# Kernel tuning notes

Hardware: AMD Instinct MI355X
Metric: run time of the kernel (lower is better)

Reference implementation:

```python
import jax, jax.numpy as jnp
import numpy as np

EMBED = 512
HEADS = 8
DIM_HEAD = 64          # embed_dim // 8
LANDMARKS = 256        # embed_dim // 2
PINV_ITERS = 6
RES_K = 33             # nystrom residual_conv_kernel default
SCALE = DIM_HEAD ** -0.5


def layer_norm(x, g, b, eps=1e-5):
    mu = x.mean(-1, keepdims=True)
    var = ((x - mu) ** 2).mean(-1, keepdims=True)
    return (x - mu) / jnp.sqrt(var + eps) * g + b


def moore_penrose_pinv(x, iters=PINV_ITERS):
    # iterative Moore-Penrose pseudo-inverse (lucidrains nystrom-attention)
    ax = jnp.abs(x)
    z = jnp.swapaxes(x, -1, -2) / (ax.sum(-1).max() * ax.sum(-2).max())
    I = jnp.eye(x.shape[-1], dtype=x.dtype)
    for _ in range(iters):
        xz = x @ z
        z = 0.25 * z @ (13. * I - xz @ (15. * I - xz @ (7. * I - xz)))
    return z


def nystrom_attention(x, w_qkv, w_out, b_out, res_k):
    b, n, _ = x.shape
    m = LANDMARKS
    pad = (m - n % m) % m
    xp = jnp.pad(x, ((0, 0), (pad, 0), (0, 0)))  # left-pad like F.pad(..., padding, 0)
    np_ = n + pad
    qkv = (xp @ w_qkv).reshape(b, np_, 3, HEADS, DIM_HEAD)
    q = qkv[:, :, 0].transpose(0, 2, 1, 3) * SCALE   # [b,h,np,dh]
    k = qkv[:, :, 1].transpose(0, 2, 1, 3)
    v = qkv[:, :, 2].transpose(0, 2, 1, 3)
    l = np_ // m
    q_l = q.reshape(b, HEADS, m, l, DIM_HEAD).mean(3)  # [b,h,m,dh]
    k_l = k.reshape(b, HEADS, m, l, DIM_HEAD).mean(3)
    attn1 = jax.nn.softmax(jnp.einsum('bhid,bhjd->bhij', q, k_l), -1)    # [b,h,np,m]
    attn2 = jax.nn.softmax(jnp.einsum('bhid,bhjd->bhij', q_l, k_l), -1)  # [b,h,m,m]
    attn3 = jax.nn.softmax(jnp.einsum('bhid,bhjd->bhij', q_l, k), -1)    # [b,h,m,np]
    out = (attn1 @ moore_penrose_pinv(attn2)) @ (attn3 @ v)              # [b,h,np,dh]
    # depthwise residual conv over the sequence dim, per head (shared across dh)
    v_c = v.transpose(0, 3, 1, 2).reshape(b * DIM_HEAD, HEADS, np_)
    res = jax.lax.conv_general_dilated(
        v_c, res_k[:, None, :], (1,), [(RES_K // 2, RES_K // 2)],
        dimension_numbers=('NCH', 'OIH', 'NCH'), feature_group_count=HEADS)
    out = out + res.reshape(b, DIM_HEAD, HEADS, np_).transpose(0, 2, 3, 1)
    out = out.transpose(0, 2, 1, 3).reshape(b, np_, HEADS * DIM_HEAD)
    out = out @ w_out + b_out
    return out[:, -n:]  # drop left padding


def dwconv2d(x, w, b, k):
    # x: [B,C,H,W], w: [C,1,k,k] depthwise
    y = jax.lax.conv_general_dilated(
        x, w, (1, 1), [(k // 2, k // 2)] * 2,
        dimension_numbers=('NCHW', 'OIHW', 'NCHW'), feature_group_count=x.shape[1])
    return y + b[None, :, None, None]


def ppeg(x, H, W, w7, b7, w5, b5, w3, b3):
    B, _, C = x.shape
    cls_tok, feat = x[:, :1], x[:, 1:]
    f = feat.transpose(0, 2, 1).reshape(B, C, H, W)
    y = f + dwconv2d(f, w7, b7, 7) + dwconv2d(f, w5, b5, 5) + dwconv2d(f, w3, b3, 3)
    y = y.reshape(B, C, H * W).transpose(0, 2, 1)
    return jnp.concatenate([cls_tok, y], axis=1)


def reference(h, w_fc1, b_fc1, cls_token,
              ln1_g, ln1_b, qkv1_w, out1_w, out1_b, res1_k,
              conv7_w, conv7_b, conv5_w, conv5_b, conv3_w, conv3_b,
              ln2_g, ln2_b, qkv2_w, out2_w, out2_b, res2_k,
              lnf_g, lnf_b):
    h = jax.nn.relu(h @ w_fc1 + b_fc1)                 # [B,N,512]
    B, N, C = h.shape
    _H = int(np.ceil(np.sqrt(N)))
    add = _H * _H - N
    h = jnp.concatenate([h, h[:, :add]], axis=1)       # square padding
    h = jnp.concatenate([jnp.broadcast_to(cls_token, (B, 1, C)), h], axis=1)
    h = h + nystrom_attention(layer_norm(h, ln1_g, ln1_b), qkv1_w, out1_w, out1_b, res1_k)
    h = ppeg(h, _H, _H, conv7_w, conv7_b, conv5_w, conv5_b, conv3_w, conv3_b)
    h = h + nystrom_attention(layer_norm(h, ln2_g, ln2_b), qkv2_w, out2_w, out2_b, res2_k)
    return layer_norm(h, lnf_g, lnf_b)[:, 0]           # [B,512]


def setup_inputs() -> dict:
    key = jax.random.key(0)
    ks = jax.random.split(key, 24)
    B, N, IN_DIM = 2, 4096, 1024
    w = lambda k, shape, s=0.02: jax.random.normal(k, shape, jnp.float32) * s
    z = lambda shape: jnp.zeros(shape, jnp.float32)
    o = lambda shape: jnp.ones(shape, jnp.float32)
    return {
        'h': jax.random.normal(ks[0], (B, N, IN_DIM), jnp.float32),
        'w_fc1': w(ks[1], (IN_DIM, EMBED)), 'b_fc1': z((EMBED,)),
        'cls_token': w(ks[2], (1, 1, EMBED)),
        'ln1_g': o((EMBED,)), 'ln1_b': z((EMBED,)),
        'qkv1_w': w(ks[3], (EMBED, 3 * HEADS * DIM_HEAD)),
        'out1_w': w(ks[4], (HEADS * DIM_HEAD, EMBED)), 'out1_b': z((EMBED,)),
        'res1_k': w(ks[5], (HEADS, RES_K), 0.1),
        'conv7_w': w(ks[6], (EMBED, 1, 7, 7), 0.05), 'conv7_b': z((EMBED,)),
        'conv5_w': w(ks[7], (EMBED, 1, 5, 5), 0.05), 'conv5_b': z((EMBED,)),
        'conv3_w': w(ks[8], (EMBED, 1, 3, 3), 0.05), 'conv3_b': z((EMBED,)),
        'ln2_g': o((EMBED,)), 'ln2_b': z((EMBED,)),
        'qkv2_w': w(ks[9], (EMBED, 3 * HEADS * DIM_HEAD)),
        'out2_w': w(ks[10], (HEADS * DIM_HEAD, EMBED)), 'out2_b': z((EMBED,)),
        'res2_k': w(ks[11], (HEADS, RES_K), 0.1),
        'lnf_g': o((EMBED,)), 'lnf_b': z((EMBED,)),
    }
```

## Files before the change

### kernel.cpp

```cpp
#include <hip/hip_runtime.h>
#include <hip/hip_bf16.h>

#define HEADS 8
#define DH 64
#define EMB 512
#define NP 4352
#define NTOK 4097
#define PADF 255
#define LM 256
#define SCALE 0.125f

typedef __attribute__((ext_vector_type(8))) short bf8;
typedef __attribute__((ext_vector_type(4))) float f4;
typedef __attribute__((ext_vector_type(8))) unsigned short us8;
typedef __attribute__((ext_vector_type(4))) unsigned short us4;
typedef unsigned short u16;

__device__ __forceinline__ u16 f2b(float f){
  union { float f; unsigned u; } x; x.f = f;
  unsigned r = x.u + 0x7fffu + ((x.u>>16)&1u);
  return (u16)(r>>16);
}
__device__ __forceinline__ float b2f(u16 h){
  union { unsigned u; float f; } x; x.u = ((unsigned)h)<<16;
  return x.f;
}

__device__ __forceinline__ void gload_lds(const u16* g, u16* l){
  __builtin_amdgcn_global_load_lds((const __attribute__((address_space(1))) void*)g,
                                   (__attribute__((address_space(3))) void*)l, 16, 0, 0);
}

template<int MODE>
__global__ __launch_bounds__(256)
void k_g128(const u16* __restrict__ A, const u16* __restrict__ B,
            float* __restrict__ C, u16* __restrict__ C16,
            int K, int lda, int ldb, int ldc,
            long sAb, long sAh, long sBb, long sBh, long sCb, long sCh, int nh,
            float alpha, const float* __restrict__ bias, int relu, int rowoff,
            int nx, int ksplit)
{
  int z = blockIdx.z;
  const u16* Ab = A + (long)(z/nh)*sAb + (long)(z%nh)*sAh;
  const u16* Bb = B + (long)(z/nh)*sBb + (long)(z%nh)*sBh;
  long cb = (long)(z/nh)*sCb + (long)(z%nh)*sCh;
  int bx = blockIdx.x % nx, kc = blockIdx.x / nx;
  int m0 = blockIdx.y*128, n0 = bx*128;
  int klen = K/ksplit, kbeg = kc*klen, nch = klen/32;
  __shared__ u16 As[2][4096];
  __shared__ u16 Bs[2][4096];
  int tid=threadIdx.x, w=tid>>6, lane=tid&63, q=lane>>4, lr=lane&15;
  int wrow=(w>>1)*64, wcol=(w&1)*64;
  int srow = tid>>2, scol = (tid&3)*8;
  const u16* ga  = Ab + (long)(m0+srow)*lda + kbeg + scol;
  const u16* ga2 = Ab + (long)(m0+64+srow)*lda + kbeg + scol;
  const u16* gb  = Bb + (long)(n0+srow)*ldb + kbeg + scol;
  const u16* gb2 = Bb + (long)(n0+64+srow)*ldb + kbeg + scol;
  int lo = srow*32 + scol;
  f4 acc[4][4] = {};
  auto stage = [&](int r, int c){
    gload_lds(ga  + c*32, &As[r][lo]);
    gload_lds(ga2 + c*32, &As[r][2048+lo]);
    gload_lds(gb  + c*32, &Bs[r][lo]);
    gload_lds(gb2 + c*32, &Bs[r][2048+lo]);
  };
  auto compute = [&](int r){
    bf8 af[4], bfr[4];
    #pragma unroll
    for(int rr=0;rr<4;rr++) af[rr]  = *(const bf8*)&As[r][(wrow + rr*16 + lr)*32 + q*8];
    #pragma unroll
    for(int t=0;t<4;t++) bfr[t] = *(const bf8*)&Bs[r][(wcol + t*16 + lr)*32 + q*8];
    #pragma unroll
    for(int rr=0;rr<4;rr++)
      #pragma unroll
      for(int t=0;t<4;t++)
        acc[rr][t] = __builtin_amdgcn_mfma_f32_16x16x32_bf16(af[rr], bfr[t], acc[rr][t], 0,0,0);
  };
  stage(0,0);
  __syncthreads();
  for(int c=1;c<nch;c++){
    stage(c&1, c);
    compute((c-1)&1);
    __syncthreads();
  }
  compute((nch-1)&1);
  #pragma unroll
  for(int r=0;r<4;r++){
    #pragma unroll
    for(int t=0;t<4;t++){
      #pragma unroll
      for(int e=0;e<4;e++){
        int gm = m0 + wrow + r*16 + q*4 + e;
        int gn = n0 + wcol + t*16 + lr;
        float v = acc[r][t][e]*alpha;
        if(MODE==4){
          if(bias && kc==0) v += bias[gn];
          if(gm>=rowoff) atomicAdd(&C[cb + (long)(gm-rowoff)*ldc + gn], v);
        } else {
          if(bias) v += bias[gn];
          if(relu) v = fmaxf(v,0.f);
          if(MODE==0) C[cb + (long)gm*ldc + gn] = v;
          else if(MODE==2) C16[cb + (long)gm*ldc + gn] = f2b(v);
          else { if(gm>=rowoff) C[cb + (long)(gm-rowoff)*ldc + gn] += v; }
        }
      }
    }
  }
}

template<int MODE>
__global__ __launch_bounds__(256)
void k_g64(const u16* __restrict__ A, const u16* __restrict__ B,
           float* __restrict__ C, u16* __restrict__ C16,
           int K, int lda, int ldb, int ldc,
           long sAb, long sAh, long sBb, long sBh, long sCb, long sCh, int nh,
           float alpha, const float* __restrict__ bias, int rowoff, int moff,
           int nx, int ksplit)
{
  int z = blockIdx.z;
  const u16* Ab = A + (long)(z/nh)*sAb + (long)(z%nh)*sAh;
  const u16* Bb = B + (long)(z/nh)*sBb + (long)(z%nh)*sBh;
  long cb = (long)(z/nh)*sCb + (long)(z%nh)*sCh;
  int bx = blockIdx.x % nx, kc = blockIdx.x / nx;
  int m0 = blockIdx.y*64 + moff, n0 = bx*64;
  int klen = K/ksplit, kbeg = kc*klen, nch = klen/32;
  __shared__ u16 As[2][2048];
  __shared__ u16 Bs[2][2048];
  int tid=threadIdx.x, w=tid>>6, lane=tid&63, q=lane>>4, lr=lane&15;
  int srow = tid>>2, scol = (tid&3)*8;
  const u16* ga = Ab + (long)(m0+srow)*lda + kbeg + scol;
  const u16* gb = Bb + (long)(n0+srow)*ldb + kbeg + scol;
  int lo = srow*32 + scol;
  f4 acc[4] = {};
  auto stage = [&](int r, int c){
    gload_lds(ga + c*32, &As[r][lo]);
    gload_lds(gb + c*32, &Bs[r][lo]);
  };
  auto compute = [&](int r){
    bf8 af = *(const bf8*)&As[r][(w*16 + lr)*32 + q*8];
    #pragma unroll
    for(int t=0;t<4;t++){
      bf8 bfr = *(const bf8*)&Bs[r][(t*16 + lr)*32 + q*8];
      acc[t] = __builtin_amdgcn_mfma_f32_16x16x32_bf16(af, bfr, acc[t], 0,0,0);
    }
  };
  stage(0,0);
  __syncthreads();
  for(int c=1;c<nch;c++){
    stage(c&1, c);
    compute((c-1)&1);
    __syncthreads();
  }
  compute((nch-1)&1);
  #pragma unroll
  for(int t=0;t<4;t++){
    #pragma unroll
    for(int e=0;e<4;e++){
      int gm = m0 + w*16 + q*4 + e;
      int gn = n0 + t*16 + lr;
      float v = acc[t][e]*alpha;
      if(MODE==0) C[cb + (long)gm*ldc + gn] = v;
      else if(MODE==2) C16[cb + (long)gm*ldc + gn] = f2b(v);
      else if(MODE==3) atomicAdd(&C[cb + (long)gm*ldc + gn], v);
      else if(MODE==5){
        v += bias[gn];
        if(gm>=rowoff) C[cb + (long)(gm-rowoff)*ldc + gn] += v;
      }
    }
  }
}

__global__ __launch_bounds__(256)
void k_pg3(const u16* __restrict__ Ah, const u16* __restrict__ Al,
           const u16* __restrict__ Bh, const u16* __restrict__ Bl,
           u16* __restrict__ Oh, u16* __restrict__ Ol, float na, float nd,
           u16* __restrict__ TOh, u16* __restrict__ TOl, float ta, float td)
{
  long zo = (long)blockIdx.z*65536;
  int m0 = blockIdx.y*32, n0 = blockIdx.x*64;
  __shared__ u16 S[2][6144];
  int tid=threadIdx.x, w=tid>>6, lane=tid&63, q=lane>>4, lr=lane&15;
  int t2 = tid & 127;
  const u16* srcA = (tid<128 ? Ah : Al) + zo + (long)(m0 + (t2>>2))*256 + (t2&3)*8;
  const u16* srcBh = Bh + zo + (long)(n0 + (tid>>2))*256 + (tid&3)*8;
  const u16* srcBl = Bl + zo + (long)(n0 + (tid>>2))*256 + (tid&3)*8;
  f4 acc[2] = {};
  auto stage = [&](int r, int c){
    gload_lds(srcA  + c*32, &S[r][tid*8]);
    gload_lds(srcBh + c*32, &S[r][2048 + tid*8]);
    gload_lds(srcBl + c*32, &S[r][4096 + tid*8]);
  };
  int mrow = (w>>1)*16 + lr;
  auto compute = [&](int r){
    bf8 ah = *(const bf8*)&S[r][mrow*32 + q*8];
    bf8 al = *(const bf8*)&S[r][1024 + mrow*32 + q*8];
    #pragma unroll
    for(int t=0;t<2;t++){
      int nrow = (w&1)*32 + t*16 + lr;
      bf8 bh = *(const bf8*)&S[r][2048 + nrow*32 + q*8];
      bf8 bl = *(const bf8*)&S[r][4096 + nrow*32 + q*8];
      acc[t] = __builtin_amdgcn_mfma_f32_16x16x32_bf16(ah, bh, acc[t], 0,0,0);
      acc[t] = __builtin_amdgcn_mfma_f32_16x16x32_bf16(ah, bl, acc[t], 0,0,0);
      acc[t] = __builtin_amdgcn_mfma_f32_16x16x32_bf16(al, bh, acc[t], 0,0,0);
    }
  };
  stage(0,0);
  __syncthreads();
  #pragma unroll
  for(int c=1;c<8;c++){
    stage(c&1, c);
    compute((c-1)&1);
    __syncthreads();
  }
  compute(1);
  #pragma unroll
  for(int t=0;t<2;t++){
    int gn = n0 + (w&1)*32 + t*16 + lr;
    if(Oh){
      #pragma unroll
      for(int r=0;r<4;r++){
        int gm = m0 + (w>>1)*16 + q*4 + r;
        float v = na*acc[t][r] + ((gm==gn)?nd:0.f);
        u16 h = f2b(v);
        long o = zo + (long)gm*256 + gn;
        Oh[o] = h; Ol[o] = f2b(v - b2f(h));
      }
    }
    if(TOh){
      us4 th, tl;
      #pragma unroll
      for(int r=0;r<4;r++){
        int gm = m0 + (w>>1)*16 + q*4 + r;
        float v = ta*acc[t][r] + ((gm==gn)?td:0.f);
        u16 h = f2b(v);
        th[r] = h; tl[r] = f2b(v - b2f(h));
      }
      long o = zo + (long)gn*256 + (m0 + (w>>1)*16 + q*4);
      *(us4*)&TOh[o] = th; *(us4*)&TOl[o] = tl;
    }
  }
}

__global__ __launch_bounds__(256)
void k_att1(const u16* __restrict__ qkv16, const u16* __restrict__ kl,
            const u16* __restrict__ zavT, float* __restrict__ Qc)
{
  int z = blockIdx.y, b = z>>3, h = z&7;
  int m0 = blockIdx.x*64;
  __shared__ u16 SQ[64*64];
  __shared__ u16 SKL[256*64];
  __shared__ u16 SZV[64*256];
  int tid=threadIdx.x, w=tid>>6, lane=tid&63, q=lane>>4, lr=lane&15;
  {
    const u16* qb = qkv16 + (long)b*NP*1536 + h*64;
    #pragma unroll
    for(int p=0;p<2;p++){
      int idx = tid + p*256; int row = idx>>3, c8 = (idx&7)*8;
      gload_lds(qb + (long)(m0+row)*1536 + c8, &SQ[row*64 + c8]);
    }
    const u16* kb = kl + (long)z*16384;
    #pragma unroll
    for(int p=0;p<8;p++){
      int idx = tid + p*256; int row = idx>>3, c8 = (idx&7)*8;
      gload_lds(kb + row*64 + c8, &SKL[row*64 + c8]);
    }
    const u16* zb = zavT + (long)z*16384;
    #pragma unroll
    for(int p=0;p<8;p++){
      int idx = tid + p*256; int row = idx>>5, c8 = (idx&31)*8;
      gload_lds(zb + row*256 + c8, &SZV[row*256 + c8]);
    }
  }
  __syncthreads();
  f4 acc[16] = {};
  {
    bf8 af0 = *(const bf8*)&SQ[(w*16+lr)*64 + q*8];
    bf8 af1 = *(const bf8*)&SQ[(w*16+lr)*64 + 32 + q*8];
    #pragma unroll
    for(int t=0;t<16;t++){
      bf8 b0 = *(const bf8*)&SKL[(t*16+lr)*64 + q*8];
      bf8 b1 = *(const bf8*)&SKL[(t*16+lr)*64 + 32 + q*8];
      acc[t] = __builtin_amdgcn_mfma_f32_16x16x32_bf16(af0, b0, acc[t], 0,0,0);
      acc[t] = __builtin_amdgcn_mfma_f32_16x16x32_bf16(af1, b1, acc[t], 0,0,0);
    }
  }
  float mx[4] = {-1e30f,-1e30f,-1e30f,-1e30f};
  #pragma unroll
  for(int t=0;t<16;t++)
    #pragma unroll
    for(int e=0;e<4;e++) mx[e] = fmaxf(mx[e], acc[t][e]*SCALE);
  #pragma unroll
  for(int s=1;s<16;s<<=1)
    #pragma unroll
    for(int e=0;e<4;e++) mx[e] = fmaxf(mx[e], __shfl_xor(mx[e], s));
  float sm[4] = {0.f,0.f,0.f,0.f};
  #pragma unroll
  for(int t=0;t<16;t++)
    #pragma unroll
    for(int e=0;e<4;e++){ float p = expf(acc[t][e]*SCALE - mx[e]); acc[t][e]=p; sm[e]+=p; }
  #pragma unroll
  for(int s=1;s<16;s<<=1)
    #pragma unroll
    for(int e=0;e<4;e++) sm[e] += __shfl_xor(sm[e], s);
  float inv[4];
  #pragma unroll
  for(int e=0;e<4;e++) inv[e] = 1.f/sm[e];
  __syncthreads();
  u16* PS = SKL;
  #pragma unroll
  for(int t=0;t<16;t++)
    #pragma unroll
    for(int e=0;e<4;e++)
      PS[(w*16 + q*4 + e)*256 + t*16 + lr] = f2b(acc[t][e]*inv[e]);
  __syncthreads();
  f4 acc2[4] = {};
  #pragma unroll
  for(int ks=0;ks<8;ks++){
    bf8 af = *(const bf8*)&PS[(w*16+lr)*256 + ks*32 + q*8];
    #pragma unroll
    for(int t=0;t<4;t++){
      bf8 bf_ = *(const bf8*)&SZV[(t*16+lr)*256 + ks*32 + q*8];
      acc2[t] = __builtin_amdgcn_mfma_f32_16x16x32_bf16(af, bf_, acc2[t], 0,0,0);
    }
  }
  #pragma unroll
  for(int t=0;t<4;t++)
    #pragma unroll
    for(int r=0;r<4;r++){
      int gm = m0 + w*16 + q*4 + r;
      int gd = t*16 + lr;
      Qc[((long)b*NP + gm)*512 + h*64 + gd] = acc2[t][r];
    }
}

__global__ __launch_bounds__(256)
void k_smw32(float* __restrict__ X){
  long row = (long)blockIdx.x*4 + (threadIdx.x>>6);
  int lane = threadIdx.x & 63;
  float* p = X + row*256;
  float4 v = *(float4*)&p[lane*4];
  float m = fmaxf(fmaxf(v.x,v.y),fmaxf(v.z,v.w));
  for(int s=32;s;s>>=1) m = fmaxf(m, __shfl_xor(m, s));
  float e0=expf(v.x-m), e1=expf(v.y-m), e2=expf(v.z-m), e3=expf(v.w-m);
  float sum = e0+e1+e2+e3;
  for(int s=32;s;s>>=1) sum += __shfl_xor(sum, s);
  float inv = 1.f/sum;
  float4 o = {e0*inv, e1*inv, e2*inv, e3*inv};
  *(float4*)&p[lane*4] = o;
}

__global__ __launch_bounds__(256)
void k_smb16(u16* __restrict__ X){
  u16* p = X + (long)blockIdx.x*4352;
  int tid=threadIdx.x, lane=tid&63, w=tid>>6;
  __shared__ float xw[4], sw[4];
  float e[17];
  float m = -1e30f;
  #pragma unroll
  for(int i=0;i<17;i++){ e[i] = b2f(p[tid + i*256]); m = fmaxf(m, e[i]); }
  for(int s=32;s;s>>=1) m = fmaxf(m, __shfl_xor(m, s));
  if(lane==0) xw[w] = m;
  __syncthreads();
  m = fmaxf(fmaxf(xw[0],xw[1]), fmaxf(xw[2],xw[3]));
  float sum = 0.f;
  #pragma unroll
  for(int i=0;i<17;i++){ e[i] = expf(e[i]-m); sum += e[i]; }
  for(int s=32;s;s>>=1) sum += __shfl_xor(sum, s);
  if(lane==0) sw[w] = sum;
  __syncthreads();
  sum = sw[0]+sw[1]+sw[2]+sw[3];
  float inv = 1.f/sum;
  #pragma unroll
  for(int i=0;i<17;i++) p[tid + i*256] = f2b(e[i]*inv);
}

__global__ void k_wT(const float* __restrict__ in, u16* __restrict__ out, int K, int N){
  int n0=blockIdx.x*32, k0=blockIdx.y*32, tid=threadIdx.x;
  __shared__ float T[32][33];
  int lr=tid&31, lc=tid>>5;
  #pragma unroll
  for(int p=0;p<4;p++) T[lc+8*p][lr] = in[(long)(k0+lc+8*p)*N + n0+lr];
  __syncthreads();
  #pragma unroll
  for(int p=0;p<4;p++) out[(long)(n0+lc+8*p)*K + k0+lr] = f2b(T[lr][lc+8*p]);
}

__global__ __launch_bounds__(256)
void k_vT(const u16* __restrict__ qkv16, u16* __restrict__ vT){
  int t0=blockIdx.x*64, h=blockIdx.y, b=blockIdx.z, tid=threadIdx.x;
  __shared__ u16 T[64][72];
  const u16* src = qkv16 + (long)b*NP*1536 + 1024 + h*64;
  for(int s=0;s<2;s++){
    int idx=tid+s*256; int row=idx>>3, c8=(idx&7)*8;
    *(us8*)&T[row][c8] = *(const us8*)&src[(long)(t0+row)*1536 + c8];
  }
  __syncthreads();
  u16* dst = vT + ((long)(b*8+h)*64)*NP;
  int d = tid>>2, j0=(tid&3)*16;
  us8 v0,v1;
  #pragma unroll
  for(int jj=0;jj<8;jj++){ v0[jj]=T[j0+jj][d]; v1[jj]=T[j0+8+jj][d]; }
  *(us8*)&dst[(long)d*NP + t0 + j0]     = v0;
  *(us8*)&dst[(long)d*NP + t0 + j0 + 8] = v1;
}

__global__ void k_cvt16(const float* __restrict__ in, u16* __restrict__ out, long n){
  long i = (long)blockIdx.x*256 + threadIdx.x;
  if(i<n) out[i] = f2b(in[i]);
}

__global__ void k_zero(float* __restrict__ p, long n){
  long i = (long)blockIdx.x*256 + threadIdx.x;
  if(i<n) p[i] = 0.f;
}

__global__ void k_cls(const float* __restrict__ cls, float* __restrict__ seq){
  int b = blockIdx.x;
  seq[(long)b*NTOK*EMB + threadIdx.x] = cls[threadIdx.x];
}

__global__ void k_ln_pad(const float* __restrict__ seq, u16* __restrict__ xp,
                         const float* __restrict__ g, const float* __restrict__ bb){
  int b = blockIdx.y, i = blockIdx.x, tid = threadIdx.x;
  u16* out = xp + ((long)b*NP + i)*EMB;
  if(i < PADF){ out[tid]=0; out[tid+256]=0; return; }
  const float* x = seq + ((long)b*NTOK + (i-PADF))*EMB;
  float v0 = x[tid], v1 = x[tid+256];
  __shared__ float red[256];
  red[tid]=v0+v1; __syncthreads();
  for(int s=128;s>0;s>>=1){ if(tid<s) red[tid]+=red[tid+s]; __syncthreads(); }
  float mu = red[0]*(1.0f/512.0f); __syncthreads();
  float d0=v0-mu, d1=v1-mu;
  red[tid]=d0*d0+d1*d1; __syncthreads();
  for(int s=128;s>0;s>>=1){ if(tid<s) red[tid]+=red[tid+s]; __syncthreads(); }
  float rstd = rsqrtf(red[0]*(1.0f/512.0f) + 1e-5f);
  out[tid]     = f2b(d0*rstd*g[tid]     + bb[tid]);
  out[tid+256] = f2b(d1*rstd*g[tid+256] + bb[tid+256]);
}

__global__ void k_landmarks(const u16* __restrict__ qkv, u16* __restrict__ q_l, u16* __restrict__ k_l){
  int j = blockIdx.x, h = blockIdx.y, b = blockIdx.z, d = threadIdx.x;
  const u16* base = qkv + (long)b*NP*1536 + h*64 + d;
  float sq=0.f, sk=0.f;
  for(int l=0;l<17;l++){
    long row = (long)(j*17+l)*1536;
    sq += b2f(base[row]);
    sk += b2f(base[row+512]);
  }
  long o = (((long)b*HEADS + h)*LM + j)*DH + d;
  q_l[o] = f2b(sq * (SCALE/17.0f));
  k_l[o] = f2b(sk * (1.0f/17.0f));
}

__global__ void k_pinv_norm(const float* __restrict__ A2, float* __restrict__ rmax, float* __restrict__ cmax){
  int z = blockIdx.x, tid = threadIdx.x;
  const float* X = A2 + (long)z*65536;
  float rs=0.f, cs=0.f;
  for(int j=0;j<256;j++){ rs += fabsf(X[tid*256+j]); cs += fabsf(X[j*256+tid]); }
  __shared__ float r1[256], r2[256];
  r1[tid]=rs; r2[tid]=cs; __syncthreads();
  for(int s=128;s>0;s>>=1){ if(tid<s){ r1[tid]=fmaxf(r1[tid],r1[tid+s]); r2[tid]=fmaxf(r2[tid],r2[tid+s]); } __syncthreads(); }
  if(tid==0){ rmax[z]=r1[0]; cmax[z]=r2[0]; }
}

__global__ void k_pair_init(const float* __restrict__ att2,
    const float* __restrict__ rmax, const float* __restrict__ cmax,
    u16* __restrict__ Xh, u16* __restrict__ Xl,
    u16* __restrict__ Zh, u16* __restrict__ Zl,
    u16* __restrict__ Zth, u16* __restrict__ Ztl)
{
  long zo = (long)blockIdx.z*65536;
  int i0 = blockIdx.y*64, j0 = blockIdx.x*64;
  float rm=0.f, cm=0.f;
  for(int t=0;t<16;t++){ rm=fmaxf(rm,rmax[t]); cm=fmaxf(cm,cmax[t]); }
  float inv = 1.0f/(rm*cm);
  __shared__ float T[64][68];
  int tid = threadIdx.x;
  int li = tid>>2, jc = (tid&3)*16;
  #pragma unroll
  for(int u=0;u<4;u++){
    float4 v = *(const float4*)&att2[zo + (long)(i0+li)*256 + j0 + jc + u*4];
    T[li][jc+u*4]=v.x; T[li][jc+u*4+1]=v.y; T[li][jc+u*4+2]=v.z; T[li][jc+u*4+3]=v.w;
    long o = zo + (long)(i0+li)*256 + j0 + jc + u*4;
    float vv[4] = {v.x,v.y,v.z,v.w};
    us4 xh, xl, zth, ztl;
    #pragma unroll
    for(int c=0;c<4;c++){
      u16 h = f2b(vv[c]); xh[c]=h; xl[c]=f2b(vv[c]-b2f(h));
      float zt = vv[c]*inv;
      u16 h2 = f2b(zt); zth[c]=h2; ztl[c]=f2b(zt-b2f(h2));
    }
    *(us4*)&Xh[o]=xh; *(us4*)&Xl[o]=xl; *(us4*)&Zth[o]=zth; *(us4*)&Ztl[o]=ztl;
  }
  __syncthreads();
  int lj = tid>>2, ic = (tid&3)*16;
  #pragma unroll
  for(int r=0;r<16;r++){
    float x = T[ic+r][lj]*inv;
    u16 h = f2b(x);
    long o = zo + (long)(j0+lj)*256 + i0 + ic + r;
    Zh[o]=h; Zl[o]=f2b(x-b2f(h));
  }
}

__global__ __launch_bounds__(256)
void k_rconv(const u16* __restrict__ qkv16, const float* __restrict__ resk,
             const float* __restrict__ Qin, u16* __restrict__ Qo16){
  int t0 = blockIdx.x*64, h = blockIdx.y, b = blockIdx.z;
  __shared__ float V[96*64];
  const u16* vb = qkv16 + (long)b*NP*1536 + 1024 + h*64;
  int tid = threadIdx.x;
  #pragma unroll
  for(int s=0;s<3;s++){
    int idx = tid + s*256;
    int row = idx>>3, c8 = (idx&7)*8;
    int p = t0 - 16 + row;
    if(p>=0 && p<NP){
      us8 v = *(const us8*)&vb[(long)p*1536 + c8];
      #pragma unroll
      for(int jj=0;jj<8;jj++) V[row*64+c8+jj] = b2f(v[jj]);
    } else {
      #pragma unroll
      for(int jj=0;jj<8;jj++) V[row*64+c8+jj] = 0.f;
    }
  }
  __syncthreads();
  int d = tid&63, lt = (tid>>6)*16;
  float acc[16] = {};
  #pragma unroll
  for(int s=0;s<48;s++){
    float val = V[(lt+s)*64 + d];
    #pragma unroll
    for(int j=0;j<16;j++){
      int tap = s - j;
      if(tap>=0 && tap<33) acc[j] += resk[h*33+tap]*val;
    }
  }
  #pragma unroll
  for(int j=0;j<16;j++){
    long idx = ((long)b*NP + t0 + lt + j)*EMB + h*64 + d;
    Qo16[idx] = f2b(Qin[idx] + acc[j]);
  }
}

__global__ __launch_bounds__(256)
void k_ppeg(const float* __restrict__ seq, float* __restrict__ out,
    const float* __restrict__ w7,const float* __restrict__ b7,
    const float* __restrict__ w5,const float* __restrict__ b5,
    const float* __restrict__ w3,const float* __restrict__ b3){
  int b = blockIdx.z, cg = blockIdx.y;
  int rp = blockIdx.x>>1, xs = blockIdx.x&1;
  int ch0 = cg*64;
  __shared__ float s7[64*49], s5[64*25], s3[64*9], sbias[64];
  int tid = threadIdx.x;
  for(int i=tid;i<64*49;i+=256) s7[i] = w7[ch0*49+i];
  for(int i=tid;i<64*25;i+=256) s5[i] = w5[ch0*25+i];
  for(int i=tid;i<64*9;i+=256)  s3[i] = w3[ch0*9+i];
  if(tid<64) sbias[tid] = b7[ch0+tid]+b5[ch0+tid]+b3[ch0+tid];
  if(cg==0 && blockIdx.x==0){
    out[(long)b*NTOK*EMB + tid]       = seq[(long)b*NTOK*EMB + tid];
    out[(long)b*NTOK*EMB + 256 + tid] = seq[(long)b*NTOK*EMB + 256 + tid];
  }
  __syncthreads();
  int c = tid & 63;
  int y = rp*4 + (tid>>6);
  const float* sbase = seq + (long)b*NTOK*EMB + EMB + (ch0 + c);
  float* obase = out + (long)b*NTOK*EMB + EMB + (ch0 + c);
  const float* W7 = &s7[c*49];
  const float* W5 = &s5[c*25];
  const float* W3 = &s3[c*9];
  float bsum = sbias[c];
  for(int xc=0;xc<4;xc++){
    int xb = xs*32 + xc*8;
    float acc[8];
    #pragma unroll
    for(int j=0;j<8;j++) acc[j] = sbase[(long)(y*64+xb+j)*EMB] + bsum;
    #pragma unroll
    for(int dy=-3;dy<=3;dy++){
      int yy = y+dy;
      if(yy<0||yy>=64) continue;
      float v[14];
      #pragma unroll
      for(int u=0;u<14;u++){
        int xx = xb + u - 3;
        v[u] = (xx>=0 && xx<64) ? sbase[(long)(yy*64+xx)*EMB] : 0.f;
      }
      #pragma unroll
      for(int dx=-3;dx<=3;dx++){
        float wsum = W7[(dy+3)*7+(dx+3)];
        if(dy>=-2&&dy<=2&&dx>=-2&&dx<=2) wsum += W5[(dy+2)*5+(dx+2)];
        if(dy>=-1&&dy<=1&&dx>=-1&&dx<=1) wsum += W3[(dy+1)*3+(dx+1)];
        #pragma unroll
        for(int j=0;j<8;j++) acc[j] += v[j+dx+3]*wsum;
      }
    }
    #pragma unroll
    for(int j=0;j<8;j++) obase[(long)(y*64+xb+j)*EMB] = acc[j];
  }
}

__global__ void k_final_ln(const float* __restrict__ seq, const float* __restrict__ g,
                           const float* __restrict__ bb, float* __restrict__ out){
  int b = blockIdx.x, tid = threadIdx.x;
  const float* x = seq + (long)b*NTOK*EMB;
  float v0 = x[tid], v1 = x[tid+256];
  __shared__ float red[256];
  red[tid]=v0+v1; __syncthreads();
  for(int s=128;s>0;s>>=1){ if(tid<s) red[tid]+=red[tid+s]; __syncthreads(); }
  float mu = red[0]*(1.0f/512.0f); __syncthreads();
  float d0=v0-mu, d1=v1-mu;
  red[tid]=d0*d0+d1*d1; __syncthreads();
  for(int s=128;s>0;s>>=1){ if(tid<s) red[tid]+=red[tid+s]; __syncthreads(); }
  float rstd = rsqrtf(red[0]*(1.0f/512.0f) + 1e-5f);
  out[b*512+tid]     = d0*rstd*g[tid]     + bb[tid];
  out[b*512+tid+256] = d1*rstd*g[tid+256] + bb[tid+256];
}

extern "C" void kernel_launch(void* const* d_in, const int* in_sizes, int n_in,
                              void* d_out, int out_size, void* d_ws, size_t ws_size,
                              hipStream_t stream) {
  const float* in[24];
  for(int i=0;i<24;i++) in[i] = (const float*)d_in[i];

  float* W = (float*)d_ws;
  size_t off = 0;
  float* seqA = W+off; off += 4195328;
  float* seqB = W+off; off += 4195328;
  float* att2 = W+off; off += 1048576;
  float* Qc   = W+off; off += 4456448;
  float* avbT = W+off; off += 262144;
  u16* xpb    = (u16*)(W+off); off += 2228224;
  u16* qkvb16 = (u16*)(W+off); off += 6684672;
  u16* vT16   = (u16*)(W+off); off += 2228224;
  u16* q_l16  = (u16*)(W+off); off += 131072;
  u16* k_l16  = (u16*)(W+off); off += 131072;
  u16* sc16   = (u16*)(W+off); off += 8912896;
  u16* avbT16 = (u16*)(W+off); off += 131072;
  u16* zavT16 = (u16*)(W+off); off += 131072;
  u16* Qc16   = (u16*)(W+off); off += 2228224;
  u16* qkvwT1 = (u16*)(W+off); off += 393216;
  u16* qkvwT2 = (u16*)(W+off); off += 393216;
  u16* outwT1 = (u16*)(W+off); off += 131072;
  u16* outwT2 = (u16*)(W+off); off += 131072;
  u16* pairs  = (u16*)(W+off); off += 9437184;
  float* rmax = W+off; off += 16;
  float* cmax = W+off; off += 16;
  if (ws_size < off*sizeof(float)) return;

  u16* h16   = sc16;
  u16* wfc1T = sc16 + 8388608;

  const long PB = 1048576;
  u16 *Xh=pairs, *Xl=pairs+PB;
  u16 *Z0h=pairs+2*PB, *Z0l=pairs+3*PB, *Z0th=pairs+4*PB, *Z0tl=pairs+5*PB;
  u16 *Z1h=pairs+6*PB, *Z1l=pairs+7*PB, *Z1th=pairs+8*PB, *Z1tl=pairs+9*PB;
  u16 *Ph=pairs+10*PB, *Pl=pairs+11*PB;
  u16 *Tth=pairs+12*PB, *Ttl=pairs+13*PB;
  u16 *Uth=pairs+14*PB, *Utl=pairs+15*PB;
  u16 *Vth=pairs+16*PB, *Vtl=pairs+17*PB;

  k_cvt16<<<32768,256,0,stream>>>(in[0], h16, 8388608L);
  k_wT<<<dim3(16,32),256,0,stream>>>(in[1],  wfc1T, 1024, 512);
  k_wT<<<dim3(48,16),256,0,stream>>>(in[6],  qkvwT1, 512, 1536);
  k_wT<<<dim3(48,16),256,0,stream>>>(in[18], qkvwT2, 512, 1536);
  k_wT<<<dim3(16,16),256,0,stream>>>(in[7],  outwT1, 512, 512);
  k_wT<<<dim3(16,16),256,0,stream>>>(in[19], outwT2, 512, 512);

  k_g128<0><<<dim3(4,32,2),256,0,stream>>>(h16, wfc1T, seqA+EMB, nullptr,
      1024, 1024,1024,512, 4194304L,0, 0,0, (long)NTOK*EMB,0, 1, 1.0f, in[2], 1, 0, 4, 1);
  k_cls<<<2,512,0,stream>>>(in[3], seqA);

  auto attention = [&](float* seq, const float* lng,const float* lnb,
                       const u16* qkvwT, const u16* outwT, const float* outb, const float* resk){
    k_ln_pad<<<dim3(NP,2),256,0,stream>>>(seq, xpb, lng, lnb);
    k_g128<2><<<dim3(12,34,2),256,0,stream>>>(xpb, qkvwT, nullptr, qkvb16,
        512, 512,512,1536, (long)NP*512,0, 0,0, (long)NP*1536,0, 1, 1.0f, nullptr, 0, 0, 12, 1);
    k_landmarks<<<dim3(LM,HEADS,2),64,0,stream>>>(qkvb16, q_l16, k_l16);
    k_vT<<<dim3(68,8,2),256,0,stream>>>(qkvb16, vT16);
    k_g128<0><<<dim3(2,2,16),256,0,stream>>>(q_l16, k_l16, att2, nullptr,
        64, 64,64,256, 0,16384, 0,16384, 0,65536, 16, 1.0f, nullptr, 0, 0, 2, 1);
    k_smw32<<<1024,256,0,stream>>>(att2);
    k_pinv_norm<<<16,256,0,stream>>>(att2, rmax, cmax);
    k_pair_init<<<dim3(4,4,16),256,0,stream>>>(att2, rmax, cmax, Xh,Xl, Z0h,Z0l, Z0th,Z0tl);
    dim3 pgrid(4,8,16);
    for(int it=0; it<6; it++){
      u16 *Zh_=(it&1)?Z1h:Z0h, *Zl_=(it&1)?Z1l:Z0l, *Zth_=(it&1)?Z1th:Z0th, *Ztl_=(it&1)?Z1tl:Z0tl;
      u16 *Nh_=(it&1)?Z0h:Z1h, *Nl_=(it&1)?Z0l:Z1l, *Nth_=(it&1)?Z0th:Z1th, *Ntl_=(it&1)?Z0tl:Z1tl;
      k_pg3<<<pgrid,256,0,stream>>>(Xh,Xl, Zth_,Ztl_, Ph,Pl,1.0f,0.f, Tth,Ttl,-1.0f,7.f);
      k_pg3<<<pgrid,256,0,stream>>>(Ph,Pl, Tth,Ttl, nullptr,nullptr,0.f,0.f, Uth,Utl,-1.0f,15.f);
      k_pg3<<<pgrid,256,0,stream>>>(Ph,Pl, Uth,Utl, nullptr,nullptr,0.f,0.f, Vth,Vtl,-1.0f,13.f);
      if(it<5) k_pg3<<<pgrid,256,0,stream>>>(Zh_,Zl_, Vth,Vtl, Nh_,Nl_,0.25f,0.f, Nth_,Ntl_,0.25f,0.f);
      else     k_pg3<<<pgrid,256,0,stream>>>(Zh_,Zl_, Vth,Vtl, Nh_,Nl_,0.25f,0.f, nullptr,nullptr,0.f,0.f);
    }
    k_g128<2><<<dim3(34,2,16),256,0,stream>>>(q_l16, qkvb16+512, nullptr, sc16,
        64, 64,1536,4352, 131072L,16384, (long)NP*1536,64, 8L*LM*NP,(long)LM*NP, 8, 1.0f, nullptr, 0, 0, 34, 1);
    k_smb16<<<4096,256,0,stream>>>(sc16);
    k_zero<<<1024,256,0,stream>>>(avbT, 262144L);
    k_g64<3><<<dim3(4*17,1,16),256,0,stream>>>(vT16, sc16, avbT, nullptr,
        4352, 4352,4352,256, 2228224L,278528L, 8L*LM*NP,(long)LM*NP, 131072L,16384L, 8, 1.0f, nullptr, 0, 0, 4, 17);
    k_cvt16<<<1024,256,0,stream>>>(avbT, avbT16, 262144L);
    k_g64<2><<<dim3(4,1,16),256,0,stream>>>(avbT16, Z0h, nullptr, zavT16,
        256, 256,256,256, 0,16384L, 0,65536L, 0,16384L, 16, 1.0f, nullptr, 0, 0, 4, 1);
    k_att1<<<dim3(68,16),256,0,stream>>>(qkvb16, k_l16, zavT16, Qc);
    k_rconv<<<dim3(68,8,2),256,0,stream>>>(qkvb16, resk, Qc, Qc16);
    k_g64<5><<<dim3(8,65,2),256,0,stream>>>(Qc16, outwT, seq, nullptr,
        512, 512,512,512, (long)NP*512,0, 0,0, (long)NTOK*EMB,0, 1, 1.0f, outb, PADF, 192, 8, 1);
  };

  attention(seqA, in[4], in[5], qkvwT1, outwT1, in[8], in[9]);
  k_ppeg<<<dim3(32,8,2),256,0,stream>>>(seqA, seqB, in[10],in[11],in[12],in[13],in[14],in[15]);
  attention(seqB, in[16], in[17], qkvwT2, outwT2, in[20], in[21]);
  k_final_ln<<<2,256,0,stream>>>(seqB, in[22], in[23], (float*)d_out);
}
```

Before: 1.039 ms.

## Fuse attn3 score, softmax and V product into split-K flash-style kernel

Replaces the materialized landmark-query × key score matrix, its separate softmax, the zeroing, the atomic-style split GEMM with V and the float-to-bf16 conversion with a single online-softmax kernel. It processes 4 key chunks in parallel per head and merges their partial results in a small merge kernel. This removes the write and re-read of the large bf16 score buffer and several launches. In exchange the fused kernel has small 128-thread blocks and a modest grid, and it adds a partial-output buffer and a merge pass. The workspace is reshuffled, and the input conversion buffers now alias the pairs region.

After: 1.025 ms. About the same (-1.4%).

```diff
diff --git a/kernel.cpp b/kernel.cpp
--- a/kernel.cpp
+++ b/kernel.cpp
@@ -241,6 +241,149 @@
   }
 }
 
+__global__ __launch_bounds__(128)
+void k_att3(const u16* __restrict__ qkv16, const u16* __restrict__ ql,
+            const u16* __restrict__ vT, float* __restrict__ partO,
+            float* __restrict__ pm, float* __restrict__ pl)
+{
+  int kc = blockIdx.x, jt = blockIdx.y, z = blockIdx.z;
+  int b = z>>3, h = z&7;
+  __shared__ u16 SQ[32*64];
+  __shared__ u16 SK[2][64*64];
+  __shared__ u16 SV[2][64*64];
+  __shared__ u16 SP[32*64];
+  int tid=threadIdx.x, w=tid>>6, lane=tid&63, q=lane>>4, lr=lane&15;
+  const u16* kb = qkv16 + (long)b*NP*1536 + 512 + h*64;
+  const u16* vb = vT + (long)z*64*NP;
+  int t00 = kc*1088;
+  {
+    const u16* qb = ql + (long)z*16384 + jt*32*64;
+    #pragma unroll
+    for(int p=0;p<2;p++){ int idx = tid + p*128; gload_lds(qb + idx*8, &SQ[idx*8]); }
+  }
+  auto stageKV = [&](int r, int i){
+    int t0 = t00 + i*64;
+    #pragma unroll
+    for(int p=0;p<4;p++){
+      int idx = tid + p*128; int row = idx>>3, c8 = (idx&7)*8;
+      gload_lds(kb + (long)(t0+row)*1536 + c8, &SK[r][idx*8]);
+      gload_lds(vb + (long)row*NP + t0 + c8, &SV[r][idx*8]);
+    }
+  };
+  stageKV(0,0);
+  __syncthreads();
+  bf8 af0 = *(const bf8*)&SQ[(w*16+lr)*64 + q*8];
+  bf8 af1 = *(const bf8*)&SQ[(w*16+lr)*64 + 32 + q*8];
+  f4 o[4] = {};
+  float m[4] = {-3e38f,-3e38f,-3e38f,-3e38f};
+  float l[4] = {0.f,0.f,0.f,0.f};
+  for(int i=0;i<17;i++){
+    int cur = i&1;
+    if(i<16) stageKV(cur^1, i+1);
+    f4 s[4] = {};
+    #pragma unroll
+    for(int t=0;t<4;t++){
+      bf8 b0 = *(const bf8*)&SK[cur][(t*16+lr)*64 + q*8];
+      bf8 b1 = *(const bf8*)&SK[cur][(t*16+lr)*64 + 32 + q*8];
+      s[t] = __builtin_amdgcn_mfma_f32_16x16x32_bf16(af0, b0, s[t], 0,0,0);
+      s[t] = __builtin_amdgcn_mfma_f32_16x16x32_bf16(af1, b1, s[t], 0,0,0);
+    }
+    float tm[4];
+    #pragma unroll
+    for(int e=0;e<4;e++) tm[e] = fmaxf(fmaxf(s[0][e],s[1][e]), fmaxf(s[2][e],s[3][e]));
+    #pragma unroll
+    for(int sh=1; sh<16; sh<<=1)
+      #pragma unroll
+      for(int e=0;e<4;e++) tm[e] = fmaxf(tm[e], __shfl_xor(tm[e], sh));
+    float rs[4];
+    #pragma unroll
+    for(int e=0;e<4;e++){
+      float mn = fmaxf(m[e], tm[e]);
+      float sc = expf(m[e]-mn);
+      m[e] = mn;
+      l[e] *= sc;
+      rs[e] = 0.f;
+      o[0][e]*=sc; o[1][e]*=sc; o[2][e]*=sc; o[3][e]*=sc;
+    }
+    #pragma unroll
+    for(int t=0;t<4;t++)
+      #pragma unroll
+      for(int e=0;e<4;e++){
+        float p = expf(s[t][e]-m[e]);
+        rs[e] += p;
+        SP[(w*16+q*4+e)*64 + t*16+lr] = f2b(p);
+      }
+    #pragma unroll
+    for(int sh=1; sh<16; sh<<=1)
+      #pragma unroll
+      for(int e=0;e<4;e++) rs[e] += __shfl_xor(rs[e], sh);
+    #pragma unroll
+    for(int e=0;e<4;e++) l[e] += rs[e];
+    #pragma unroll
+    for(int ks=0;ks<2;ks++){
+      bf8 pa = *(const bf8*)&SP[(w*16+lr)*64 + ks*32 + q*8];
+      #pragma unroll
+      for(int t2=0;t2<4;t2++){
+        bf8 vv = *(const bf8*)&SV[cur][(t2*16+lr)*64 + ks*32 + q*8];
+        o[t2] = __builtin_amdgcn_mfma_f32_16x16x32_bf16(pa, vv, o[t2], 0,0,0);
+      }
+    }
+    __syncthreads();
+  }
+  long pb = (long)(z*4+kc)*256 + jt*32 + w*16;
+  #pragma unroll
+  for(int e=0;e<4;e++){
+    int jg = q*4+e;
+    #pragma unroll
+    for(int t2=0;t2<4;t2++)
+      partO[(pb + jg)*64 + t2*16 + lr] = o[t2][e];
+    if(lr==0){ pm[pb + jg] = m[e]; pl[pb + jg] = l[e]; }
+  }
+}
+
+__global__ __launch_bounds__(128)
+void k_mrg3(const float* __restrict__ partO, const float* __restrict__ pm,
+            const float* __restrict__ pl, u16* __restrict__ avbT16)
+{
+  int jq = blockIdx.x, z = blockIdx.y, tid = threadIdx.x;
+  __shared__ float wk[64][4];
+  __shared__ u16 T[64][66];
+  if(tid < 64){
+    int j = jq*64 + tid;
+    float mm[4], ll[4];
+    #pragma unroll
+    for(int kc=0;kc<4;kc++){ mm[kc]=pm[(z*4+kc)*256 + j]; ll[kc]=pl[(z*4+kc)*256 + j]; }
+    float M = fmaxf(fmaxf(mm[0],mm[1]),fmaxf(mm[2],mm[3]));
+    float e0=expf(mm[0]-M), e1=expf(mm[1]-M), e2=expf(mm[2]-M), e3=expf(mm[3]-M);
+    float inv = 1.f/(ll[0]*e0+ll[1]*e1+ll[2]*e2+ll[3]*e3);
+    wk[tid][0]=e0*inv; wk[tid][1]=e1*inv; wk[tid][2]=e2*inv; wk[tid][3]=e3*inv;
+  }
+  __syncthreads();
+  float acc[32];
+  #pragma unroll
+  for(int p=0;p<32;p++) acc[p]=0.f;
+  for(int kc=0;kc<4;kc++){
+    long base = ((long)(z*4+kc)*256 + jq*64)*64;
+    #pragma unroll
+    for(int p=0;p<32;p++){
+      int idx = tid + p*128;
+      acc[p] += wk[idx>>6][kc]*partO[base + idx];
+    }
+  }
+  #pragma unroll
+  for(int p=0;p<32;p++){ int idx = tid + p*128; T[idx&63][idx>>6] = f2b(acc[p]); }
+  __syncthreads();
+  int d = tid>>1, jh = (tid&1)*32;
+  u16* dst = avbT16 + (long)(z*64+d)*256 + jq*64 + jh;
+  #pragma unroll
+  for(int c=0;c<4;c++){
+    us8 vv;
+    #pragma unroll
+    for(int u=0;u<8;u++) vv[u] = T[d][jh + c*8 + u];
+    *(us8*)&dst[c*8] = vv;
+  }
+}
+
 __global__ __launch_bounds__(256)
 void k_att1(const u16* __restrict__ qkv16, const u16* __restrict__ kl,
             const u16* __restrict__ zavT, float* __restrict__ Qc)
@@ -349,31 +492,6 @@
   *(float4*)&p[lane*4] = o;
 }
 
-__global__ __launch_bounds__(256)
-void k_smb16(u16* __restrict__ X){
-  u16* p = X + (long)blockIdx.x*4352;
-  int tid=threadIdx.x, lane=tid&63, w=tid>>6;
-  __shared__ float xw[4], sw[4];
-  float e[17];
-  float m = -1e30f;
-  #pragma unroll
-  for(int i=0;i<17;i++){ e[i] = b2f(p[tid + i*256]); m = fmaxf(m, e[i]); }
-  for(int s=32;s;s>>=1) m = fmaxf(m, __shfl_xor(m, s));
-  if(lane==0) xw[w] = m;
-  __syncthreads();
-  m = fmaxf(fmaxf(xw[0],xw[1]), fmaxf(xw[2],xw[3]));
-  float sum = 0.f;
-  #pragma unroll
-  for(int i=0;i<17;i++){ e[i] = expf(e[i]-m); sum += e[i]; }
-  for(int s=32;s;s>>=1) sum += __shfl_xor(sum, s);
-  if(lane==0) sw[w] = sum;
-  __syncthreads();
-  sum = sw[0]+sw[1]+sw[2]+sw[3];
-  float inv = 1.f/sum;
-  #pragma unroll
-  for(int i=0;i<17;i++) p[tid + i*256] = f2b(e[i]*inv);
-}
-
 __global__ void k_wT(const float* __restrict__ in, u16* __restrict__ out, int K, int N){
   int n0=blockIdx.x*32, k0=blockIdx.y*32, tid=threadIdx.x;
   __shared__ float T[32][33];
@@ -407,11 +525,6 @@
 __global__ void k_cvt16(const float* __restrict__ in, u16* __restrict__ out, long n){
   long i = (long)blockIdx.x*256 + threadIdx.x;
   if(i<n) out[i] = f2b(in[i]);
-}
-
-__global__ void k_zero(float* __restrict__ p, long n){
-  long i = (long)blockIdx.x*256 + threadIdx.x;
-  if(i<n) p[i] = 0.f;
 }
 
 __global__ void k_cls(const float* __restrict__ cls, float* __restrict__ seq){
@@ -628,13 +741,14 @@
   float* seqB = W+off; off += 4195328;
   float* att2 = W+off; off += 1048576;
   float* Qc   = W+off; off += 4456448;
-  float* avbT = W+off; off += 262144;
+  float* partO= W+off; off += 1048576;
+  float* pm   = W+off; off += 16384;
+  float* pl   = W+off; off += 16384;
   u16* xpb    = (u16*)(W+off); off += 2228224;
   u16* qkvb16 = (u16*)(W+off); off += 6684672;
   u16* vT16   = (u16*)(W+off); off += 2228224;
   u16* q_l16  = (u16*)(W+off); off += 131072;
   u16* k_l16  = (u16*)(W+off); off += 131072;
-  u16* sc16   = (u16*)(W+off); off += 8912896;
   u16* avbT16 = (u16*)(W+off); off += 131072;
   u16* zavT16 = (u16*)(W+off); off += 131072;
   u16* Qc16   = (u16*)(W+off); off += 2228224;
@@ -647,8 +761,8 @@
   float* cmax = W+off; off += 16;
   if (ws_size < off*sizeof(float)) return;
 
-  u16* h16   = sc16;
-  u16* wfc1T = sc16 + 8388608;
+  u16* h16   = pairs;
+  u16* wfc1T = pairs + 8388608;
 
   const long PB = 1048576;
   u16 *Xh=pairs, *Xl=pairs+PB;
@@ -692,13 +806,8 @@
       if(it<5) k_pg3<<<pgrid,256,0,stream>>>(Zh_,Zl_, Vth,Vtl, Nh_,Nl_,0.25f,0.f, Nth_,Ntl_,0.25f,0.f);
       else     k_pg3<<<pgrid,256,0,stream>>>(Zh_,Zl_, Vth,Vtl, Nh_,Nl_,0.25f,0.f, nullptr,nullptr,0.f,0.f);
     }
-    k_g128<2><<<dim3(34,2,16),256,0,stream>>>(q_l16, qkvb16+512, nullptr, sc16,
-        64, 64,1536,4352, 131072L,16384, (long)NP*1536,64, 8L*LM*NP,(long)LM*NP, 8, 1.0f, nullptr, 0, 0, 34, 1);
-    k_smb16<<<4096,256,0,stream>>>(sc16);
-    k_zero<<<1024,256,0,stream>>>(avbT, 262144L);
-    k_g64<3><<<dim3(4*17,1,16),256,0,stream>>>(vT16, sc16, avbT, nullptr,
-        4352, 4352,4352,256, 2228224L,278528L, 8L*LM*NP,(long)LM*NP, 131072L,16384L, 8, 1.0f, nullptr, 0, 0, 4, 17);
-    k_cvt16<<<1024,256,0,stream>>>(avbT, avbT16, 262144L);
+    k_att3<<<dim3(4,8,16),128,0,stream>>>(qkvb16, q_l16, vT16, partO, pm, pl);
+    k_mrg3<<<dim3(4,16),128,0,stream>>>(partO, pm, pl, avbT16);
     k_g64<2><<<dim3(4,1,16),256,0,stream>>>(avbT16, Z0h, nullptr, zavT16,
         256, 256,256,256, 0,16384L, 0,65536L, 0,16384L, 16, 1.0f, nullptr, 0, 0, 4, 1);
     k_att1<<<dim3(68,16),256,0,stream>>>(qkvb16, k_l16, zavT16, Qc);
```
